# Optimization experiments

Measured on AMD Instinct MI355X. Metric: run time of the kernel, lower is better.

The kernel has to match this reference:

```python
import jax, jax.numpy as jnp
import numpy as np

MIN_DEPTH, MAX_DEPTH = 0.1, 100.0
BN_EPS = 1e-5


def _conv(x, w, b, pad):
    y = jax.lax.conv_general_dilated(
        x, w, window_strides=(1, 1), padding=[(pad, pad), (pad, pad)],
        dimension_numbers=("NCHW", "OIHW", "NCHW"))
    return y + b[None, :, None, None]


def _bn(x, gamma, beta, mean, var):
    # eval-mode BatchNorm2d with running stats
    inv = jax.lax.rsqrt(var + BN_EPS)
    return (x - mean[None, :, None, None]) * (gamma * inv)[None, :, None, None] + beta[None, :, None, None]


def _object_depths(depth, bboxes):
    # depth: (B,1,H,W), bboxes: (B,N,4) int — per-box median (lower median, like torch)
    B, _, H, W = depth.shape
    xs = jnp.arange(W)
    ys = jnp.arange(H)

    def per_image(d2, boxes):  # d2: (H,W), boxes: (N,4)
        dflat = d2.reshape(-1)

        def one_box(box):
            x1 = jnp.maximum(box[0], 0)
            y1 = jnp.maximum(box[1], 0)
            x2 = jnp.minimum(box[2], W)
            y2 = jnp.minimum(box[3], H)
            mask = (((ys >= y1) & (ys < y2))[:, None] & ((xs >= x1) & (xs < x2))[None, :]).reshape(-1)
            vals = jnp.where(mask, dflat, jnp.inf)
            s = jnp.sort(vals)
            k = mask.sum()
            idx = jnp.maximum((k - 1) // 2, 0)
            med = jnp.take(s, idx)
            return jnp.where(k > 0, med, jnp.zeros((), dtype=d2.dtype))

        return jax.vmap(one_box)(boxes)

    return jax.vmap(per_image)(depth[:, 0], bboxes)


def _forward(features, bboxes, w1, b1, g1, be1, m1, v1, w2, b2, g2, be2, m2, v2,
             w3, b3, uw1, ub1, uw2, ub2):
    # depth head
    h = jax.nn.relu(_bn(_conv(features, w1, b1, 1), g1, be1, m1, v1))
    h = jax.nn.relu(_bn(_conv(h, w2, b2, 1), g2, be2, m2, v2))
    disp = jax.nn.sigmoid(_conv(h, w3, b3, 0))  # (B,1,H,W)
    min_disp = 1.0 / MAX_DEPTH
    max_disp = 1.0 / MIN_DEPTH
    depth = 1.0 / (min_disp + (max_disp - min_disp) * disp)
    # uncertainty head
    u = jax.nn.relu(_conv(features, uw1, ub1, 1))
    uncertainty = jax.nn.softplus(_conv(u, uw2, ub2, 0))
    obj = _object_depths(depth, bboxes)
    return depth, uncertainty, obj


def setup_inputs() -> dict:
    key = jax.random.key(0)
    ks = jax.random.split(key, 16)
    B, C, Hc, H, W, N = 8, 256, 256, 96, 160, 64
    f32 = jnp.float32
    inp = {
        "features": jax.random.normal(ks[0], (B, C, H, W), dtype=f32),
        "bboxes": jax.random.randint(ks[1], (B, N, 4), 0, 96, dtype=jnp.int32),
        "w1": jax.random.normal(ks[2], (Hc, C, 3, 3), dtype=f32) * 0.02,
        "b1": jnp.zeros((Hc,), f32),
        "g1": jnp.ones((Hc,), f32),
        "be1": jnp.zeros((Hc,), f32),
        "m1": jax.random.normal(ks[3], (Hc,), dtype=f32) * 0.1,
        "v1": jnp.ones((Hc,), f32),
        "w2": jax.random.normal(ks[4], (Hc, Hc, 3, 3), dtype=f32) * 0.02,
        "b2": jnp.zeros((Hc,), f32),
        "g2": jnp.ones((Hc,), f32),
        "be2": jnp.zeros((Hc,), f32),
        "m2": jax.random.normal(ks[5], (Hc,), dtype=f32) * 0.1,
        "v2": jnp.ones((Hc,), f32),
        "w3": jax.random.normal(ks[6], (1, Hc, 1, 1), dtype=f32) * 0.05,
        "b3": jnp.zeros((1,), f32),
        "uw1": jax.random.normal(ks[7], (Hc // 2, C, 3, 3), dtype=f32) * 0.02,
        "ub1": jnp.zeros((Hc // 2,), f32),
        "uw2": jax.random.normal(ks[8], (1, Hc // 2, 1, 1), dtype=f32) * 0.05,
        "ub2": jnp.zeros((1,), f32),
    }
    return inp


def reference(features, bboxes, w1, b1, g1, be1, m1, v1, w2, b2, g2, be2, m2, v2,
              w3, b3, uw1, ub1, uw2, ub2):
    return _forward(features, bboxes, w1, b1, g1, be1, m1, v1, w2, b2, g2, be2,
                    m2, v2, w3, b3, uw1, ub1, uw2, ub2)
```

## Files before the change

### kernel.cpp

```cpp
#include <hip/hip_runtime.h>
#include <hip/hip_bf16.h>

#define HH 96
#define WW 160
#define BATCH 8
#define NPIX (BATCH*HH*WW)
#define CIN 256
#define IMG (HH*WW)
#define PW 162
#define PH 98
#define PR (PH*PW)
#define PTOT (BATCH*PR)

typedef short bf16x8 __attribute__((ext_vector_type(8)));
typedef float f32x4 __attribute__((ext_vector_type(4)));

__device__ __forceinline__ unsigned short f2bf(float f) {
    unsigned int u = __float_as_uint(f);
    u = (u + 0x7fffu + ((u >> 16) & 1u)) >> 16;
    return (unsigned short)u;
}

__device__ __forceinline__ void gload16(const void* g, void* l) {
    __builtin_amdgcn_global_load_lds(
        (const __attribute__((address_space(1))) void*)g,
        (__attribute__((address_space(3))) void*)l,
        16, 0, 0);
}

__global__ __launch_bounds__(256) void prep_scalars(
    const float* __restrict__ b1, const float* __restrict__ g1, const float* __restrict__ be1,
    const float* __restrict__ m1, const float* __restrict__ v1,
    const float* __restrict__ b2, const float* __restrict__ g2, const float* __restrict__ be2,
    const float* __restrict__ m2, const float* __restrict__ v2,
    const float* __restrict__ ub1,
    float* __restrict__ scale1, float* __restrict__ bias1,
    float* __restrict__ scale2, float* __restrict__ bias2)
{
    int t = threadIdx.x;
    float s1 = g1[t] * rsqrtf(v1[t] + 1e-5f);
    scale1[t] = s1;
    bias1[t]  = (b1[t] - m1[t]) * s1 + be1[t];
    float s2 = g2[t] * rsqrtf(v2[t] + 1e-5f);
    scale2[t] = s2;
    bias2[t]  = (b2[t] - m2[t]) * s2 + be2[t];
    if (t < 128) { scale1[256 + t] = 1.0f; bias1[256 + t] = ub1[t]; }
}

__global__ __launch_bounds__(256) void prep_weights(
    const float* __restrict__ w1, const float* __restrict__ w2, const float* __restrict__ uw1,
    unsigned short* __restrict__ w1T, unsigned short* __restrict__ w2T, unsigned short* __restrict__ uw1T)
{
    const int S = 256 * 2304;
    int i = blockIdx.x * 256 + threadIdx.x;
    if (i < S) {
        int co = i / 2304, r = i % 2304, pos = r >> 8, ci = r & 255;
        w1T[i] = f2bf(w1[(co * 256 + ci) * 9 + pos]);
    } else if (i < 2 * S) {
        int j = i - S;
        int co = j / 2304, r = j % 2304, pos = r >> 8, ci = r & 255;
        w2T[j] = f2bf(w2[(co * 256 + ci) * 9 + pos]);
    } else {
        int j = i - 2 * S;
        int co = j / 2304, r = j % 2304, pos = r >> 8, ci = r & 255;
        uw1T[j] = f2bf(uw1[(co * 256 + ci) * 9 + pos]);
    }
}

__global__ __launch_bounds__(128) void zero_pads(
    unsigned int* __restrict__ featP, unsigned int* __restrict__ h1P)
{
    int bid = blockIdx.x;
    unsigned int* buf = (bid < 4128) ? featP : h1P;
    int k = (bid < 4128) ? bid : (bid - 4128);
    int img = k / 516, i = k % 516;
    int py, px;
    if (i < PW)            { py = 0;      px = i; }
    else if (i < 2 * PW)   { py = PH - 1; px = i - PW; }
    else { int q = i - 2 * PW; py = 1 + (q >> 1); px = (q & 1) ? (PW - 1) : 0; }
    size_t row = (size_t)img * PR + (size_t)py * PW + px;
    buf[row * 128 + threadIdx.x] = 0;
}

__global__ __launch_bounds__(256) void pack_features(
    const float* __restrict__ f, unsigned short* __restrict__ ft)
{
    __shared__ float tile[32][33];
    int x0 = blockIdx.x * 32;
    int c0 = blockIdx.y * 32;
    int by = blockIdx.z;
    int b = by / HH, y = by % HH;
    int tx = threadIdx.x & 31, tg = threadIdx.x >> 5;
    const float* src = f + (((size_t)(b * CIN + c0) * HH + y) * WW) + x0;
    #pragma unroll
    for (int i = 0; i < 4; ++i) {
        int cl = tg + i * 8;
        tile[cl][tx] = src[(size_t)cl * HH * WW + tx];
    }
    __syncthreads();
    size_t rbase = (size_t)b * PR + (size_t)(y + 1) * PW + (x0 + 1);
    #pragma unroll
    for (int i = 0; i < 4; ++i) {
        int xl = tg + i * 8;
        ft[(rbase + xl) * 256 + c0 + tx] = f2bf(tile[tx][xl]);
    }
}

__global__ __launch_bounds__(256) void conv3x3_mfma(
    const unsigned short* __restrict__ inP,
    const unsigned short* __restrict__ wT,
    const float* __restrict__ scale, const float* __restrict__ bias,
    unsigned short* __restrict__ outT,
    float* __restrict__ uout,
    const float* __restrict__ uw2, const float* __restrict__ ub2,
    int Cout, int mode, int My)
{
    __shared__ unsigned short Alds[3 * 128 * 32];
    __shared__ unsigned short Blds[144 * 32];
    __shared__ float usum[2][128];

    const int t = threadIdx.x;
    const int wave = t >> 6;
    const int l = t & 63;

    const int lid = blockIdx.x;
    const int xcd = lid & 7;
    const int j = lid >> 3;
    const int n0 = (xcd * 120 + j / My) * 128;
    const int m0 = (j % My) * 128;
    const bool is_unc = (mode == 1) && (m0 == 256);

    const int b0 = n0 / IMG;
    const int rem0 = n0 % IMG;
    const int y0 = rem0 / WW;
    const int x0 = rem0 % WW;
    const int r0 = b0 * PR + (y0 + 1) * PW + (x0 + 1);

    const int lrow = l >> 2;
    const int lkq = (l & 3) ^ ((l >> 3) & 3);

    const unsigned short* asrc0 = wT + (size_t)(m0 + wave * 32 + lrow) * 9 * 256 + lkq * 8;
    const unsigned short* asrc1 = asrc0 + (size_t)16 * 9 * 256;

    char* AldsB = (char*)Alds;
    char* BldsB = (char*)Blds;
    char* aldst = AldsB + wave * 2048;

    const int wm = wave >> 1, wn = wave & 1;
    const int quad = l >> 4, lane16 = l & 15;
    const int aoff = lane16 * 64 + ((quad ^ ((lane16 >> 1) & 3)) << 4);

    int browbase[4];
    #pragma unroll
    for (int i = 0; i < 4; ++i) {
        int jj = wn * 64 + i * 16 + lane16;
        browbase[i] = jj + ((x0 + jj) >= WW ? 2 : 0) + 7;
    }

    f32x4 acc[4][4];
    #pragma unroll
    for (int mt = 0; mt < 4; ++mt)
        #pragma unroll
        for (int nt = 0; nt < 4; ++nt)
            acc[mt][nt] = (f32x4){0.f, 0.f, 0.f, 0.f};

    for (int cc = 0; cc < 8; ++cc) {
        const int ccoff = cc * 32;
        for (int dyi = 0; dyi < 3; ++dyi) {
            __syncthreads();
            const unsigned short* a0 = asrc0 + (dyi * 3) * 256 + ccoff;
            const unsigned short* a1 = asrc1 + (dyi * 3) * 256 + ccoff;
            #pragma unroll
            for (int dxp = 0; dxp < 3; ++dxp) {
                gload16(a0 + dxp * 256, aldst + dxp * 8192);
                gload16(a1 + dxp * 256, aldst + dxp * 8192 + 1024);
            }
            const ptrdiff_t rs = (ptrdiff_t)r0 + (ptrdiff_t)(dyi - 1) * PW - 8;
            const unsigned short* bs = inP + (rs + lrow) * 256 + ccoff + lkq * 8
                                           + (size_t)wave * 8192;
            gload16(bs, BldsB + wave * 2048);
            gload16(bs + 4096, BldsB + wave * 2048 + 1024);
            if (wave == 3) gload16(bs + 8192, BldsB + 8192);
            __syncthreads();
            #pragma unroll
            for (int dx = 0; dx < 3; ++dx) {
                bf16x8 af[4], bfr[4];
                #pragma unroll
                for (int mt = 0; mt < 4; ++mt)
                    af[mt] = *(const bf16x8*)(AldsB + dx * 8192 + ((wm * 4 + mt) << 10) + aoff);
                #pragma unroll
                for (int i = 0; i < 4; ++i) {
                    int row = browbase[i] + dx;
                    int ba = (row << 6) + ((quad ^ ((row >> 1) & 3)) << 4);
                    bfr[i] = *(const bf16x8*)(BldsB + ba);
                }
                #pragma unroll
                for (int mt = 0; mt < 4; ++mt)
                    #pragma unroll
                    for (int nt = 0; nt < 4; ++nt)
                        acc[mt][nt] = __builtin_amdgcn_mfma_f32_16x16x32_bf16(
                            af[mt], bfr[nt], acc[mt][nt], 0, 0, 0);
            }
        }
    }

    if (is_unc) {
        const float* ub = bias + 256;
        float s[4] = {0.f, 0.f, 0.f, 0.f};
        #pragma unroll
        for (int mt = 0; mt < 4; ++mt) {
            const int mg = wm * 64 + mt * 16 + quad * 4;
            const float4 bi = *(const float4*)&ub[mg];
            const float4 uw = *(const float4*)&uw2[mg];
            #pragma unroll
            for (int nt = 0; nt < 4; ++nt) {
                s[nt] += fmaxf(acc[mt][nt][0] + bi.x, 0.f) * uw.x
                       + fmaxf(acc[mt][nt][1] + bi.y, 0.f) * uw.y
                       + fmaxf(acc[mt][nt][2] + bi.z, 0.f) * uw.z
                       + fmaxf(acc[mt][nt][3] + bi.w, 0.f) * uw.w;
            }
        }
        #pragma unroll
        for (int nt = 0; nt < 4; ++nt) {
            s[nt] += __shfl_xor(s[nt], 16);
            s[nt] += __shfl_xor(s[nt], 32);
        }
        if (quad == 0) {
            #pragma unroll
            for (int nt = 0; nt < 4; ++nt)
                usum[wm][wn * 64 + nt * 16 + lane16] = s[nt];
        }
        __syncthreads();
        if (t < 128) {
            float x = usum[0][t] + usum[1][t] + ub2[0];
            uout[n0 + t] = fmaxf(x, 0.f) + log1pf(expf(-fabsf(x)));
        }
        return;
    }

    size_t obase[4];
    #pragma unroll
    for (int nt = 0; nt < 4; ++nt) {
        int n = n0 + wn * 64 + nt * 16 + lane16;
        if (mode == 1) {
            int b = n / IMG, rem = n % IMG, yy = rem / WW, xx = rem % WW;
            obase[nt] = ((size_t)(b * PH + yy + 1) * PW + (xx + 1)) * 256;
        } else {
            obase[nt] = (size_t)n * Cout;
        }
    }
    #pragma unroll
    for (int mt = 0; mt < 4; ++mt) {
        const int mg = m0 + wm * 64 + mt * 16 + quad * 4;
        const float4 sc = *(const float4*)&scale[mg];
        const float4 bi = *(const float4*)&bias[mg];
        #pragma unroll
        for (int nt = 0; nt < 4; ++nt) {
            ushort4 pk;
            pk.x = f2bf(fmaxf(acc[mt][nt][0] * sc.x + bi.x, 0.f));
            pk.y = f2bf(fmaxf(acc[mt][nt][1] * sc.y + bi.y, 0.f));
            pk.z = f2bf(fmaxf(acc[mt][nt][2] * sc.z + bi.z, 0.f));
            pk.w = f2bf(fmaxf(acc[mt][nt][3] * sc.w + bi.w, 0.f));
            *(ushort4*)&outT[obase[nt] + mg] = pk;
        }
    }
}

__global__ __launch_bounds__(256) void head_depth(
    const unsigned short* __restrict__ h2, const float* __restrict__ w3,
    const float* __restrict__ b3, float* __restrict__ out)
{
    __shared__ float ws[256];
    ws[threadIdx.x] = w3[threadIdx.x];
    __syncthreads();
    const int pix = blockIdx.x * 64 + (threadIdx.x >> 2);
    const int q = threadIdx.x & 3;
    const unsigned short* p = h2 + (size_t)pix * 256 + q * 64;
    float s = 0.f;
    #pragma unroll
    for (int i = 0; i < 64; i += 8) {
        uint4 v = *(const uint4*)(p + i);
        const float* wq = &ws[q * 64 + i];
        s += __uint_as_float(v.x << 16) * wq[0];
        s += __uint_as_float(v.x & 0xffff0000u) * wq[1];
        s += __uint_as_float(v.y << 16) * wq[2];
        s += __uint_as_float(v.y & 0xffff0000u) * wq[3];
        s += __uint_as_float(v.z << 16) * wq[4];
        s += __uint_as_float(v.z & 0xffff0000u) * wq[5];
        s += __uint_as_float(v.w << 16) * wq[6];
        s += __uint_as_float(v.w & 0xffff0000u) * wq[7];
    }
    s += __shfl_xor(s, 1);
    s += __shfl_xor(s, 2);
    if (q == 0) {
        float x = s + b3[0];
        float sig = 1.f / (1.f + expf(-x));
        out[pix] = 1.f / (0.01f + 9.99f * sig);
    }
}

__global__ __launch_bounds__(256) void median_kernel(
    const float* __restrict__ depth, const int* __restrict__ bboxes, float* __restrict__ obj)
{
    const int bi = blockIdx.x;
    const int b = bi >> 6;
    const int* bb = bboxes + (size_t)bi * 4;
    int x1 = max(bb[0], 0), y1 = max(bb[1], 0);
    int x2 = min(bb[2], WW), y2 = min(bb[3], HH);
    int w = x2 - x1, h = y2 - y1;
    if (w <= 0 || h <= 0) {
        if (threadIdx.x == 0) obj[bi] = 0.f;
        return;
    }
    const int wh = w * h;
    int tgt = (wh - 1) >> 1;
    const float* dbase = depth + (size_t)b * HH * WW;

    __shared__ unsigned int hist[256];
    __shared__ unsigned int sel_prefix, sel_target;
    unsigned int prefix = 0;

    for (int pass = 0; pass < 4; ++pass) {
        const int shift = 24 - 8 * pass;
        hist[threadIdx.x] = 0;
        __syncthreads();
        const unsigned int mask_high = (pass == 0) ? 0u : (0xFFFFFFFFu << (shift + 8));
        for (int idx = threadIdx.x; idx < wh; idx += 256) {
            int yy = y1 + idx / w, xx = x1 + idx % w;
            unsigned int uu = __float_as_uint(dbase[yy * WW + xx]);
            if ((uu & mask_high) == (prefix & mask_high))
                atomicAdd(&hist[(uu >> shift) & 255], 1u);
        }
        __syncthreads();
        if (threadIdx.x == 0) {
            unsigned int cum = 0;
            for (int bin = 0; bin < 256; ++bin) {
                unsigned int c = hist[bin];
                if (cum + c > (unsigned int)tgt) {
                    sel_target = (unsigned int)tgt - cum;
                    sel_prefix = prefix | ((unsigned int)bin << shift);
                    break;
                }
                cum += c;
            }
        }
        __syncthreads();
        prefix = sel_prefix;
        tgt = (int)sel_target;
    }
    if (threadIdx.x == 0) obj[bi] = __uint_as_float(prefix);
}

extern "C" void kernel_launch(void* const* d_in, const int* in_sizes, int n_in,
                              void* d_out, int out_size, void* d_ws, size_t ws_size,
                              hipStream_t stream) {
    const float* features = (const float*)d_in[0];
    const int*   bboxes   = (const int*)d_in[1];
    const float* w1  = (const float*)d_in[2];
    const float* b1  = (const float*)d_in[3];
    const float* g1  = (const float*)d_in[4];
    const float* be1 = (const float*)d_in[5];
    const float* m1  = (const float*)d_in[6];
    const float* v1  = (const float*)d_in[7];
    const float* w2  = (const float*)d_in[8];
    const float* b2  = (const float*)d_in[9];
    const float* g2  = (const float*)d_in[10];
    const float* be2 = (const float*)d_in[11];
    const float* m2  = (const float*)d_in[12];
    const float* v2  = (const float*)d_in[13];
    const float* w3  = (const float*)d_in[14];
    const float* b3  = (const float*)d_in[15];
    const float* uw1 = (const float*)d_in[16];
    const float* ub1 = (const float*)d_in[17];
    const float* uw2 = (const float*)d_in[18];
    const float* ub2 = (const float*)d_in[19];
    float* out = (float*)d_out;

    char* ws = (char*)d_ws;
    unsigned short* featP = (unsigned short*)(ws + 8192);
    unsigned short* h1P   = (unsigned short*)(ws + 65044480);
    unsigned short* h2    = (unsigned short*)(ws + 8192);
    unsigned short* w1T   = (unsigned short*)(ws + 130080768);
    unsigned short* uw1T  = w1T + 256 * 2304;
    unsigned short* w2T   = uw1T + 128 * 2304;
    float* scale1 = (float*)(w2T + 589824);
    float* bias1  = scale1 + 384;
    float* scale2 = bias1 + 384;
    float* bias2  = scale2 + 256;

    prep_scalars<<<1, 256, 0, stream>>>(b1, g1, be1, m1, v1, b2, g2, be2, m2, v2, ub1,
                                        scale1, bias1, scale2, bias2);
    prep_weights<<<5760, 256, 0, stream>>>(w1, w2, uw1, w1T, w2T, uw1T);
    zero_pads<<<8256, 128, 0, stream>>>((unsigned int*)featP, (unsigned int*)h1P);
    pack_features<<<dim3(WW / 32, CIN / 32, BATCH * HH), 256, 0, stream>>>(features, featP);

    conv3x3_mfma<<<2880, 256, 0, stream>>>(
        featP, w1T, scale1, bias1, h1P, out + NPIX, uw2, ub2, 256, 1, 3);
    conv3x3_mfma<<<1920, 256, 0, stream>>>(
        h1P, w2T, scale2, bias2, h2, nullptr, nullptr, nullptr, 256, 0, 2);

    head_depth<<<NPIX / 64, 256, 0, stream>>>(h2, w3, b3, out);
    median_kernel<<<BATCH * 64, 256, 0, stream>>>(out, bboxes, out + 2 * NPIX);
}
```

Baseline: 677.2 us.

## Double-buffer conv3x3 MFMA LDS tiles with manual vmcnt waits and barriers

Converts the conv3x3 MFMA main loop from a single LDS buffer, with two full syncthreads per step, into a two-stage ping-pong pipeline. The next (channel-chunk, dy) slice is issued via global_load_lds while the current slice is being computed. Partial s_waitcnt vmcnt counts leave the prefetch in flight, and s_setprio raises priority around the MFMA block. This doubles the LDS footprint, which may reduce occupancy, and the hand-counted vmcnt values must match exactly the loads each wave issues.

```diff
diff --git a/kernel.cpp b/kernel.cpp
--- a/kernel.cpp
+++ b/kernel.cpp
@@ -115,8 +115,8 @@
     const float* __restrict__ uw2, const float* __restrict__ ub2,
     int Cout, int mode, int My)
 {
-    __shared__ unsigned short Alds[3 * 128 * 32];
-    __shared__ unsigned short Blds[144 * 32];
+    __shared__ unsigned short Alds[2][3 * 128 * 32];
+    __shared__ unsigned short Blds[2][144 * 32];
     __shared__ float usum[2][128];
 
     const int t = threadIdx.x;
@@ -144,7 +144,6 @@
 
     char* AldsB = (char*)Alds;
     char* BldsB = (char*)Blds;
-    char* aldst = AldsB + wave * 2048;
 
     const int wm = wave >> 1, wn = wave & 1;
     const int quad = l >> 4, lane16 = l & 15;
@@ -164,44 +163,67 @@
         for (int nt = 0; nt < 4; ++nt)
             acc[mt][nt] = (f32x4){0.f, 0.f, 0.f, 0.f};
 
-    for (int cc = 0; cc < 8; ++cc) {
-        const int ccoff = cc * 32;
-        for (int dyi = 0; dyi < 3; ++dyi) {
-            __syncthreads();
-            const unsigned short* a0 = asrc0 + (dyi * 3) * 256 + ccoff;
-            const unsigned short* a1 = asrc1 + (dyi * 3) * 256 + ccoff;
+    auto STAGE = [&](int ccoff, int dyi, int sel) {
+        const unsigned short* a0 = asrc0 + (dyi * 3) * 256 + ccoff;
+        const unsigned short* a1 = asrc1 + (dyi * 3) * 256 + ccoff;
+        char* ad = AldsB + sel * 24576 + wave * 2048;
+        #pragma unroll
+        for (int dxp = 0; dxp < 3; ++dxp) {
+            gload16(a0 + dxp * 256, ad + dxp * 8192);
+            gload16(a1 + dxp * 256, ad + dxp * 8192 + 1024);
+        }
+        const ptrdiff_t rs = (ptrdiff_t)r0 + (ptrdiff_t)(dyi - 1) * PW - 8;
+        const unsigned short* bs = inP + (rs + lrow) * 256 + ccoff + lkq * 8
+                                       + (size_t)wave * 8192;
+        char* bd = BldsB + sel * 9216;
+        gload16(bs, bd + wave * 2048);
+        gload16(bs + 4096, bd + wave * 2048 + 1024);
+        if (wave == 3) gload16(bs + 8192, bd + 8192);
+    };
+
+    STAGE(0, 0, 0);
+
+    int cur = 0;
+    int ccoffN = 0, dyiN = 1;
+    for (int it = 0; it < 24; ++it) {
+        if (it < 23) {
+            STAGE(ccoffN, dyiN, cur ^ 1);
+            if (++dyiN == 3) { dyiN = 0; ccoffN += 32; }
+            if (wave == 3) { asm volatile("s_waitcnt vmcnt(9)" ::: "memory"); }
+            else           { asm volatile("s_waitcnt vmcnt(8)" ::: "memory"); }
+        } else {
+            asm volatile("s_waitcnt vmcnt(0)" ::: "memory");
+        }
+        __builtin_amdgcn_s_barrier();
+        asm volatile("" ::: "memory");
+
+        __builtin_amdgcn_s_setprio(1);
+        const char* Ab = AldsB + cur * 24576;
+        const char* Bb = BldsB + cur * 9216;
+        #pragma unroll
+        for (int dx = 0; dx < 3; ++dx) {
+            bf16x8 af[4], bfr[4];
             #pragma unroll
-            for (int dxp = 0; dxp < 3; ++dxp) {
-                gload16(a0 + dxp * 256, aldst + dxp * 8192);
-                gload16(a1 + dxp * 256, aldst + dxp * 8192 + 1024);
+            for (int mt = 0; mt < 4; ++mt)
+                af[mt] = *(const bf16x8*)(Ab + dx * 8192 + ((wm * 4 + mt) << 10) + aoff);
+            #pragma unroll
+            for (int i = 0; i < 4; ++i) {
+                int row = browbase[i] + dx;
+                int ba = (row << 6) + ((quad ^ ((row >> 1) & 3)) << 4);
+                bfr[i] = *(const bf16x8*)(Bb + ba);
             }
-            const ptrdiff_t rs = (ptrdiff_t)r0 + (ptrdiff_t)(dyi - 1) * PW - 8;
-            const unsigned short* bs = inP + (rs + lrow) * 256 + ccoff + lkq * 8
-                                           + (size_t)wave * 8192;
-            gload16(bs, BldsB + wave * 2048);
-            gload16(bs + 4096, BldsB + wave * 2048 + 1024);
-            if (wave == 3) gload16(bs + 8192, BldsB + 8192);
-            __syncthreads();
             #pragma unroll
-            for (int dx = 0; dx < 3; ++dx) {
-                bf16x8 af[4], bfr[4];
+            for (int mt = 0; mt < 4; ++mt)
                 #pragma unroll
-                for (int mt = 0; mt < 4; ++mt)
-                    af[mt] = *(const bf16x8*)(AldsB + dx * 8192 + ((wm * 4 + mt) << 10) + aoff);
-                #pragma unroll
-                for (int i = 0; i < 4; ++i) {
-                    int row = browbase[i] + dx;
-                    int ba = (row << 6) + ((quad ^ ((row >> 1) & 3)) << 4);
-                    bfr[i] = *(const bf16x8*)(BldsB + ba);
-                }
-                #pragma unroll
-                for (int mt = 0; mt < 4; ++mt)
-                    #pragma unroll
-                    for (int nt = 0; nt < 4; ++nt)
-                        acc[mt][nt] = __builtin_amdgcn_mfma_f32_16x16x32_bf16(
-                            af[mt], bfr[nt], acc[mt][nt], 0, 0, 0);
-            }
-        }
+                for (int nt = 0; nt < 4; ++nt)
+                    acc[mt][nt] = __builtin_amdgcn_mfma_f32_16x16x32_bf16(
+                        af[mt], bfr[nt], acc[mt][nt], 0, 0, 0);
+        }
+        __builtin_amdgcn_s_setprio(0);
+
+        asm volatile("" ::: "memory");
+        __builtin_amdgcn_s_barrier();
+        cur ^= 1;
     }
 
     if (is_unc) {
```

New measurement: 658.7 us. 2.7% less time.
